# Optimization experiments

Measured on AMD Instinct MI355X. Metric: run time of the kernel, lower is better.

## Reference

```python
import jax, jax.numpy as jnp
import numpy as np

N_NODES = 100000


def setup_inputs() -> dict:
    key = jax.random.key(0)
    k1, k2, k3, k4, k5, k6 = jax.random.split(key, 6)
    n_edges = 1600000
    X = jax.random.normal(k1, (N_NODES, 256), dtype=jnp.float32)
    edge_row = jax.random.randint(k2, (n_edges,), 0, N_NODES, dtype=jnp.int64)
    edge_col = jax.random.randint(k3, (n_edges,), 0, N_NODES, dtype=jnp.int64)
    edge_val = jax.random.uniform(k4, (n_edges,), dtype=jnp.float32)
    W = jax.random.normal(k5, (128, 256), dtype=jnp.float32) * 0.05
    b = jax.random.normal(k6, (128,), dtype=jnp.float32) * 0.05
    return {"X": X, "edge_row": edge_row, "edge_col": edge_col,
            "edge_val": edge_val, "W": W, "b": b}


def reference(X, edge_row, edge_col, edge_val, W, b):
    # Dense projection: H = X @ W^T + b  -> [N, out_dim]
    H = jnp.einsum('ni,oi->no', X, W) + b
    # SpMM: out[r] = sum_e A[r, c_e] * H[c_e] over edges with row r
    msgs = edge_val[:, None] * H[edge_col]          # [E, out_dim]
    out = jax.ops.segment_sum(msgs, edge_row, num_segments=N_NODES)
    return out
```

## Files before the change

kernel.cpp:

```cpp
#include <hip/hip_runtime.h>
#include <hip/hip_bf16.h>

#define NNODES 100000
#define NEDGES 1600000
#define KDIM 256
#define ODIM 128
#define NSHARD 16
#define NB_SCAN 391
#define EDGE_CAP 1900032
#define ESTRIDE 400000
#define GEMM_BLOCKS 1563
#define RANK_BLOCKS 1563

typedef __attribute__((ext_vector_type(8))) short short8;
typedef __attribute__((ext_vector_type(4))) float floatx4;

static __device__ __forceinline__ short f2bf(float f) {
  union { float f; unsigned u; } x; x.f = f;
  unsigned r = (x.u + 0x7fffu + ((x.u >> 16) & 1u)) >> 16;
  return (short)r;
}

__global__ void conv_w_kernel(const float* __restrict__ W, short* __restrict__ Wb) {
  int i = blockIdx.x * 256 + threadIdx.x;
  if (i < ODIM * KDIM) Wb[i] = f2bf(W[i]);
}

__global__ void scan1_kernel(const int* __restrict__ counts, int* __restrict__ chunkExcl,
                             int* __restrict__ blockSums) {
  __shared__ int s[256];
  int t = threadIdx.x;
  int n = blockIdx.x * 256 + t;
  int sum = 0;
  if (n < NNODES) {
    const int4* c4 = (const int4*)(counts + (size_t)n * NSHARD);
    int4 a = c4[0], b = c4[1], c = c4[2], d = c4[3];
    sum = a.x + a.y + a.z + a.w + b.x + b.y + b.z + b.w +
          c.x + c.y + c.z + c.w + d.x + d.y + d.z + d.w;
    sum = (sum + 3) & ~3;
  }
  s[t] = sum;
  __syncthreads();
  for (int o = 1; o < 256; o <<= 1) {
    int add = (t >= o) ? s[t - o] : 0;
    __syncthreads();
    s[t] += add;
    __syncthreads();
  }
  if (n < NNODES) chunkExcl[n] = s[t] - sum;
  if (t == 255) blockSums[blockIdx.x] = s[255];
}

__global__ void scan2_kernel(const int* __restrict__ blockSums, int* __restrict__ blockBase,
                             int* __restrict__ offsets) {
  __shared__ int s[512];
  int t = threadIdx.x;
  int v = (t < NB_SCAN) ? blockSums[t] : 0;
  s[t] = v;
  __syncthreads();
  for (int o = 1; o < 512; o <<= 1) {
    int add = (t >= o) ? s[t - o] : 0;
    __syncthreads();
    s[t] += add;
    __syncthreads();
  }
  if (t < NB_SCAN) blockBase[t] = s[t] - v;
  if (t == 511) offsets[NNODES] = s[511];
}

__global__ void scan3_kernel(const int* __restrict__ chunkExcl, const int* __restrict__ blockBase,
                             int* __restrict__ counts, int* __restrict__ offsets) {
  int n = blockIdx.x * 256 + threadIdx.x;
  if (n >= NNODES) return;
  int run = chunkExcl[n] + blockBase[n >> 8];
  offsets[n] = run;
  int4* c4 = (int4*)(counts + (size_t)n * NSHARD);
  int4 q0 = c4[0], q1 = c4[1], q2 = c4[2], q3 = c4[3];
  int4 b0, b1, b2, b3;
  b0.x = run; run += q0.x; b0.y = run; run += q0.y;
  b0.z = run; run += q0.z; b0.w = run; run += q0.w;
  b1.x = run; run += q1.x; b1.y = run; run += q1.y;
  b1.z = run; run += q1.z; b1.w = run; run += q1.w;
  b2.x = run; run += q2.x; b2.y = run; run += q2.y;
  b2.z = run; run += q2.z; b2.w = run; run += q2.w;
  b3.x = run; run += q3.x; b3.y = run; run += q3.y;
  b3.z = run; run += q3.z; b3.w = run; run += q3.w;
  c4[0] = b0; c4[1] = b1; c4[2] = b2; c4[3] = b3;
}

__global__ void place_kernel(const int* __restrict__ rows, const int* __restrict__ cols,
                             const float* __restrict__ vals,
                             const unsigned short* __restrict__ rank,
                             const int* __restrict__ sbase, int2* __restrict__ edges) {
  int i = blockIdx.x * 256 + threadIdx.x;
#pragma unroll
  for (int j = 0; j < 4; j++) {
    int e = i + j * ESTRIDE;
    if (e < NEDGES) {
      int r = rows[e];
      int p = sbase[(r << 4) | (e & 15)] + (int)rank[e];
      int2 rec;
      rec.x = cols[e];
      rec.y = __float_as_int(vals[e]);
      edges[p] = rec;
    }
  }
}

__global__ __launch_bounds__(256) void gemm_rank_kernel(
    const float* __restrict__ X, const short* __restrict__ Wb,
    const float* __restrict__ bias, unsigned* __restrict__ H2,
    const int* __restrict__ rows, int* __restrict__ counts,
    unsigned short* __restrict__ rank) {
  if (blockIdx.x >= GEMM_BLOCKS) {
    int i = (blockIdx.x - GEMM_BLOCKS) * 256 + threadIdx.x;
#pragma unroll
    for (int j = 0; j < 4; j++) {
      int e = i + j * ESTRIDE;
      if (e < NEDGES) {
        int r = rows[e];
        rank[e] = (unsigned short)atomicAdd(&counts[(r << 4) | (e & 15)], 1);
      }
    }
    return;
  }
  const int lane = threadIdx.x & 63;
  const int wave = threadIdx.x >> 6;
  const int l16 = lane & 15;
  const int quad = lane >> 4;
  const int rowBase = blockIdx.x * 64 + wave * 16;
  const int arow = rowBase + l16;
  const bool inb = arow < NNODES;
  const float4 zf4 = {0.f, 0.f, 0.f, 0.f};
  const float4* xp = (const float4*)(X + (size_t)(inb ? arow : 0) * KDIM + quad * 8);

  float4 xr[16];
#pragma unroll
  for (int k0 = 0; k0 < 8; k0++) {
    xr[2 * k0]     = inb ? xp[k0 * 8]     : zf4;
    xr[2 * k0 + 1] = inb ? xp[k0 * 8 + 1] : zf4;
  }

  floatx4 acc[8];
#pragma unroll
  for (int t = 0; t < 8; t++) acc[t] = (floatx4){0.f, 0.f, 0.f, 0.f};

#pragma unroll
  for (int k0 = 0; k0 < 8; k0++) {
    const float4 c0 = xr[2 * k0];
    const float4 c1 = xr[2 * k0 + 1];
    short8 a;
    a[0] = f2bf(c0.x); a[1] = f2bf(c0.y); a[2] = f2bf(c0.z); a[3] = f2bf(c0.w);
    a[4] = f2bf(c1.x); a[5] = f2bf(c1.y); a[6] = f2bf(c1.z); a[7] = f2bf(c1.w);
    const short* bp = Wb + k0 * 32 + quad * 8;
#pragma unroll
    for (int t = 0; t < 8; t++) {
      short8 b = *(const short8*)(bp + (size_t)(t * 16 + l16) * KDIM);
      acc[t] = __builtin_amdgcn_mfma_f32_16x16x32_bf16(a, b, acc[t], 0, 0, 0);
    }
  }

#pragma unroll
  for (int t = 0; t < 4; t++) {
    const int cl = t * 16 + l16;
    const float blo = bias[cl];
    const float bhi = bias[cl + 64];
#pragma unroll
    for (int r = 0; r < 4; r++) {
      const int row = rowBase + quad * 4 + r;
      if (row < NNODES) {
        unsigned lo = (unsigned short)f2bf(acc[t][r] + blo);
        unsigned hi = (unsigned short)f2bf(acc[t + 4][r] + bhi);
        H2[(size_t)row * 64 + cl] = lo | (hi << 16);
      }
    }
  }
}

__global__ __launch_bounds__(256) void spmm_kernel(const int* __restrict__ offsets,
                                                   const int2* __restrict__ edges,
                                                   const unsigned* __restrict__ H2,
                                                   float* __restrict__ out) {
  const int lane = threadIdx.x & 63;
  const int row = blockIdx.x * 4 + (threadIdx.x >> 6);
  if (row >= NNODES) return;
  const int s = offsets[row];
  const int e = offsets[row + 1];
  float ax = 0.f, ay = 0.f;
  for (int i = s; i < e; i += 4) {
    const int4 p01 = *(const int4*)(edges + i);
    const int4 p23 = *(const int4*)(edges + i + 2);
    const unsigned h0 = H2[(size_t)p01.x * 64 + lane];
    const unsigned h1 = H2[(size_t)p01.z * 64 + lane];
    const unsigned h2 = H2[(size_t)p23.x * 64 + lane];
    const unsigned h3 = H2[(size_t)p23.z * 64 + lane];
    const float v0 = __int_as_float(p01.y);
    const float v1 = __int_as_float(p01.w);
    const float v2 = __int_as_float(p23.y);
    const float v3 = __int_as_float(p23.w);
    ax += v0 * __uint_as_float(h0 << 16);
    ay += v0 * __uint_as_float(h0 & 0xffff0000u);
    ax += v1 * __uint_as_float(h1 << 16);
    ay += v1 * __uint_as_float(h1 & 0xffff0000u);
    ax += v2 * __uint_as_float(h2 << 16);
    ay += v2 * __uint_as_float(h2 & 0xffff0000u);
    ax += v3 * __uint_as_float(h3 << 16);
    ay += v3 * __uint_as_float(h3 & 0xffff0000u);
  }
  out[(size_t)row * 128 + lane] = ax;
  out[(size_t)row * 128 + 64 + lane] = ay;
}

extern "C" void kernel_launch(void* const* d_in, const int* in_sizes, int n_in,
                              void* d_out, int out_size, void* d_ws, size_t ws_size,
                              hipStream_t stream) {
  const float* X = (const float*)d_in[0];
  const int* erow = (const int*)d_in[1];
  const int* ecol = (const int*)d_in[2];
  const float* eval = (const float*)d_in[3];
  const float* W = (const float*)d_in[4];
  const float* bias = (const float*)d_in[5];
  float* out = (float*)d_out;

  char* ws = (char*)d_ws;
  size_t off = 0;
  auto alloc = [&](size_t bytes) -> char* {
    char* p = ws + off;
    off += (bytes + 255) & ~(size_t)255;
    return p;
  };
  unsigned* Hb = (unsigned*)alloc((size_t)NNODES * 64 * 4);
  short* Wb = (short*)alloc((size_t)ODIM * KDIM * 2);
  int* counts = (int*)alloc((size_t)NNODES * NSHARD * 4);
  int* chunkExcl = (int*)alloc((size_t)NNODES * 4);
  int* offsets = (int*)alloc((size_t)(NNODES + 1) * 4);
  int* blockSums = (int*)alloc((size_t)NB_SCAN * 4);
  int* blockBase = (int*)alloc((size_t)NB_SCAN * 4);
  unsigned short* rank = (unsigned short*)alloc((size_t)NEDGES * 2);
  int2* edges = (int2*)alloc((size_t)EDGE_CAP * 8);

  hipMemsetAsync(counts, 0, (size_t)NNODES * NSHARD * 4, stream);
  hipMemsetAsync(edges, 0, (size_t)EDGE_CAP * 8, stream);
  conv_w_kernel<<<(ODIM * KDIM + 255) / 256, 256, 0, stream>>>(W, Wb);
  gemm_rank_kernel<<<GEMM_BLOCKS + RANK_BLOCKS, 256, 0, stream>>>(X, Wb, bias, Hb,
                                                                 erow, counts, rank);
  scan1_kernel<<<NB_SCAN, 256, 0, stream>>>(counts, chunkExcl, blockSums);
  scan2_kernel<<<1, 512, 0, stream>>>(blockSums, blockBase, offsets);
  scan3_kernel<<<NB_SCAN, 256, 0, stream>>>(chunkExcl, blockBase, counts, offsets);
  place_kernel<<<(ESTRIDE + 255) / 256, 256, 0, stream>>>(erow, ecol, eval, rank, counts, edges);
  spmm_kernel<<<(NNODES + 3) / 4, 256, 0, stream>>>(offsets, edges, (const unsigned*)Hb, out);
}
```

Baseline: 437.8 us.

## Shard degree counters per XCD with workgroup-scope atomics and prefetch X in GEMM

Replaces the 16-way edge-index sharded degree counters with one counter array per XCD, read from the XCC_ID hardware register. Increments now use relaxed, workgroup-scope atomics, and the XCD id is packed into the high byte of each edge's rank. The goal is to keep atomic traffic local to each XCD's L2 and to shrink the counter layout, which the scan and place kernels now read as [8][N] planes. Rank blocks are moved ahead of GEMM blocks in the fused launch. The GEMM now software-prefetches the next X slice instead of loading the whole row up front, which lowers register pressure. The risks are correctness if workgroup-scope atomics are not coherent across CUs within an XCD, and rank overflow if more than 255 edges of one row land on a single XCD.

```diff
diff --git a/kernel.cpp b/kernel.cpp
--- a/kernel.cpp
+++ b/kernel.cpp
@@ -5,7 +5,7 @@
 #define NEDGES 1600000
 #define KDIM 256
 #define ODIM 128
-#define NSHARD 16
+#define NXCD 8
 #define NB_SCAN 391
 #define EDGE_CAP 1900032
 #define ESTRIDE 400000
@@ -26,18 +26,17 @@
   if (i < ODIM * KDIM) Wb[i] = f2bf(W[i]);
 }
 
-__global__ void scan1_kernel(const int* __restrict__ counts, int* __restrict__ chunkExcl,
+__global__ void scan1_kernel(const unsigned* __restrict__ counts, int* __restrict__ chunkExcl,
                              int* __restrict__ blockSums) {
   __shared__ int s[256];
   int t = threadIdx.x;
   int n = blockIdx.x * 256 + t;
   int sum = 0;
   if (n < NNODES) {
-    const int4* c4 = (const int4*)(counts + (size_t)n * NSHARD);
-    int4 a = c4[0], b = c4[1], c = c4[2], d = c4[3];
-    sum = a.x + a.y + a.z + a.w + b.x + b.y + b.z + b.w +
-          c.x + c.y + c.z + c.w + d.x + d.y + d.z + d.w;
-    sum = (sum + 3) & ~3;
+    int s0 = 0;
+#pragma unroll
+    for (int x = 0; x < NXCD; x++) s0 += (int)counts[(size_t)x * NNODES + n];
+    sum = (s0 + 3) & ~3;
   }
   s[t] = sum;
   __syncthreads();
@@ -69,36 +68,31 @@
 }
 
 __global__ void scan3_kernel(const int* __restrict__ chunkExcl, const int* __restrict__ blockBase,
-                             int* __restrict__ counts, int* __restrict__ offsets) {
+                             unsigned* __restrict__ counts, int* __restrict__ offsets) {
   int n = blockIdx.x * 256 + threadIdx.x;
   if (n >= NNODES) return;
   int run = chunkExcl[n] + blockBase[n >> 8];
   offsets[n] = run;
-  int4* c4 = (int4*)(counts + (size_t)n * NSHARD);
-  int4 q0 = c4[0], q1 = c4[1], q2 = c4[2], q3 = c4[3];
-  int4 b0, b1, b2, b3;
-  b0.x = run; run += q0.x; b0.y = run; run += q0.y;
-  b0.z = run; run += q0.z; b0.w = run; run += q0.w;
-  b1.x = run; run += q1.x; b1.y = run; run += q1.y;
-  b1.z = run; run += q1.z; b1.w = run; run += q1.w;
-  b2.x = run; run += q2.x; b2.y = run; run += q2.y;
-  b2.z = run; run += q2.z; b2.w = run; run += q2.w;
-  b3.x = run; run += q3.x; b3.y = run; run += q3.y;
-  b3.z = run; run += q3.z; b3.w = run; run += q3.w;
-  c4[0] = b0; c4[1] = b1; c4[2] = b2; c4[3] = b3;
+#pragma unroll
+  for (int x = 0; x < NXCD; x++) {
+    int c = (int)counts[(size_t)x * NNODES + n];
+    counts[(size_t)x * NNODES + n] = (unsigned)run;
+    run += c;
+  }
 }
 
 __global__ void place_kernel(const int* __restrict__ rows, const int* __restrict__ cols,
                              const float* __restrict__ vals,
                              const unsigned short* __restrict__ rank,
-                             const int* __restrict__ sbase, int2* __restrict__ edges) {
+                             const unsigned* __restrict__ sbase, int2* __restrict__ edges) {
   int i = blockIdx.x * 256 + threadIdx.x;
 #pragma unroll
   for (int j = 0; j < 4; j++) {
     int e = i + j * ESTRIDE;
     if (e < NEDGES) {
       int r = rows[e];
-      int p = sbase[(r << 4) | (e & 15)] + (int)rank[e];
+      unsigned rk = rank[e];
+      int p = (int)sbase[(size_t)(rk >> 8) * NNODES + r] + (int)(rk & 255u);
       int2 rec;
       rec.x = cols[e];
       rec.y = __float_as_int(vals[e]);
@@ -110,45 +104,50 @@
 __global__ __launch_bounds__(256) void gemm_rank_kernel(
     const float* __restrict__ X, const short* __restrict__ Wb,
     const float* __restrict__ bias, unsigned* __restrict__ H2,
-    const int* __restrict__ rows, int* __restrict__ counts,
+    const int* __restrict__ rows, unsigned* __restrict__ counts,
     unsigned short* __restrict__ rank) {
-  if (blockIdx.x >= GEMM_BLOCKS) {
-    int i = (blockIdx.x - GEMM_BLOCKS) * 256 + threadIdx.x;
+  if (blockIdx.x < RANK_BLOCKS) {
+    unsigned xcc;
+    asm("s_getreg_b32 %0, hwreg(HW_REG_XCC_ID)" : "=s"(xcc));
+    xcc &= 7u;
+    unsigned* cbase = counts + (size_t)xcc * NNODES;
+    int i = blockIdx.x * 256 + threadIdx.x;
 #pragma unroll
     for (int j = 0; j < 4; j++) {
       int e = i + j * ESTRIDE;
       if (e < NEDGES) {
         int r = rows[e];
-        rank[e] = (unsigned short)atomicAdd(&counts[(r << 4) | (e & 15)], 1);
+        unsigned old = __hip_atomic_fetch_add(&cbase[r], 1u, __ATOMIC_RELAXED,
+                                              __HIP_MEMORY_SCOPE_WORKGROUP);
+        rank[e] = (unsigned short)((xcc << 8) | old);
       }
     }
     return;
   }
+  const int gb = blockIdx.x - RANK_BLOCKS;
   const int lane = threadIdx.x & 63;
   const int wave = threadIdx.x >> 6;
   const int l16 = lane & 15;
   const int quad = lane >> 4;
-  const int rowBase = blockIdx.x * 64 + wave * 16;
+  const int rowBase = gb * 64 + wave * 16;
   const int arow = rowBase + l16;
   const bool inb = arow < NNODES;
   const float4 zf4 = {0.f, 0.f, 0.f, 0.f};
   const float4* xp = (const float4*)(X + (size_t)(inb ? arow : 0) * KDIM + quad * 8);
 
-  float4 xr[16];
+  floatx4 acc[8];
+#pragma unroll
+  for (int t = 0; t < 8; t++) acc[t] = (floatx4){0.f, 0.f, 0.f, 0.f};
+
+  float4 c0 = inb ? xp[0] : zf4;
+  float4 c1 = inb ? xp[1] : zf4;
 #pragma unroll
   for (int k0 = 0; k0 < 8; k0++) {
-    xr[2 * k0]     = inb ? xp[k0 * 8]     : zf4;
-    xr[2 * k0 + 1] = inb ? xp[k0 * 8 + 1] : zf4;
-  }
-
-  floatx4 acc[8];
-#pragma unroll
-  for (int t = 0; t < 8; t++) acc[t] = (floatx4){0.f, 0.f, 0.f, 0.f};
-
-#pragma unroll
-  for (int k0 = 0; k0 < 8; k0++) {
-    const float4 c0 = xr[2 * k0];
-    const float4 c1 = xr[2 * k0 + 1];
+    float4 n0, n1;
+    if (k0 < 7) {
+      n0 = inb ? xp[(k0 + 1) * 8] : zf4;
+      n1 = inb ? xp[(k0 + 1) * 8 + 1] : zf4;
+    }
     short8 a;
     a[0] = f2bf(c0.x); a[1] = f2bf(c0.y); a[2] = f2bf(c0.z); a[3] = f2bf(c0.w);
     a[4] = f2bf(c1.x); a[5] = f2bf(c1.y); a[6] = f2bf(c1.z); a[7] = f2bf(c1.w);
@@ -158,6 +157,7 @@
       short8 b = *(const short8*)(bp + (size_t)(t * 16 + l16) * KDIM);
       acc[t] = __builtin_amdgcn_mfma_f32_16x16x32_bf16(a, b, acc[t], 0, 0, 0);
     }
+    if (k0 < 7) { c0 = n0; c1 = n1; }
   }
 
 #pragma unroll
@@ -231,7 +231,7 @@
   };
   unsigned* Hb = (unsigned*)alloc((size_t)NNODES * 64 * 4);
   short* Wb = (short*)alloc((size_t)ODIM * KDIM * 2);
-  int* counts = (int*)alloc((size_t)NNODES * NSHARD * 4);
+  unsigned* counts = (unsigned*)alloc((size_t)NXCD * NNODES * 4);
   int* chunkExcl = (int*)alloc((size_t)NNODES * 4);
   int* offsets = (int*)alloc((size_t)(NNODES + 1) * 4);
   int* blockSums = (int*)alloc((size_t)NB_SCAN * 4);
@@ -239,11 +239,11 @@
   unsigned short* rank = (unsigned short*)alloc((size_t)NEDGES * 2);
   int2* edges = (int2*)alloc((size_t)EDGE_CAP * 8);
 
-  hipMemsetAsync(counts, 0, (size_t)NNODES * NSHARD * 4, stream);
+  hipMemsetAsync(counts, 0, (size_t)NXCD * NNODES * 4, stream);
   hipMemsetAsync(edges, 0, (size_t)EDGE_CAP * 8, stream);
   conv_w_kernel<<<(ODIM * KDIM + 255) / 256, 256, 0, stream>>>(W, Wb);
-  gemm_rank_kernel<<<GEMM_BLOCKS + RANK_BLOCKS, 256, 0, stream>>>(X, Wb, bias, Hb,
-                                                                 erow, counts, rank);
+  gemm_rank_kernel<<<RANK_BLOCKS + GEMM_BLOCKS, 256, 0, stream>>>(X, Wb, bias, Hb,
+                                                                  erow, counts, rank);
   scan1_kernel<<<NB_SCAN, 256, 0, stream>>>(counts, chunkExcl, blockSums);
   scan2_kernel<<<1, 512, 0, stream>>>(blockSums, blockBase, offsets);
   scan3_kernel<<<NB_SCAN, 256, 0, stream>>>(chunkExcl, blockBase, counts, offsets);
```

Result: faster. 403.7 us (-7.8%).
